# Optimization experiments

Hardware: AMD Instinct MI355X
Metric: run time of the kernel (lower is better)

Reference implementation:

```python
import jax, jax.numpy as jnp
import numpy as np

B, H, W = 8, 512, 512


def _focal_row_loss(logits, t):
    # logits: [B,2,H,W], t: [B,H,W] float. lossweight hardcoded to 1 as in source.
    logp = jax.nn.log_softmax(logits, axis=1)
    p = jnp.exp(logp)
    l = (-t * jnp.square(1.0 - p[:, 1]) * logp[:, 1]
         - (1.0 - t) * jnp.square(1.0 - p[:, 0]) * logp[:, 0])
    return l.reshape(l.shape[0], -1), p, logp


def _forward(inputs1, inputs2, inputs3, targets, forget_rate, kdweight):
    bsz = targets.shape[0]
    t = targets.astype(jnp.float32)
    loss_1, p1, lp1 = _focal_row_loss(inputs1, t)
    loss_2, p2, lp2 = _focal_row_loss(inputs2, t)
    loss_3, p3, lp3 = _focal_row_loss(inputs3, t)

    # symmetric per-pixel KL between the two class distributions (stable via log-softmax diff)
    kdl_12 = (p1[:, 0] * (lp1[:, 0] - lp2[:, 0]) + p1[:, 1] * (lp1[:, 1] - lp2[:, 1])).reshape(bsz, -1)
    kdl_21 = (p2[:, 0] * (lp2[:, 0] - lp1[:, 0]) + p2[:, 1] * (lp2[:, 1] - lp1[:, 1])).reshape(bsz, -1)

    loss = (1.0 - kdweight) * (loss_1 + loss_2 + loss_3) + kdweight * (kdl_12 + kdl_21)

    remember_rate = 1.0 - forget_rate
    num_remember = int(remember_rate * loss_1.shape[1])  # static: forget_rate is a Python float

    # on-device per-row top-(num_remember) smallest-loss pixels, then batched gather from loss_3
    ind_sorted = jnp.argsort(loss, axis=1)            # [B, N]
    ind_update = ind_sorted[:, :num_remember]          # [B, num_remember]
    loss_update = jnp.take_along_axis(loss_3, ind_update, axis=1)  # [B, num_remember]

    loss_out = jnp.mean(loss_update)  # reduction='mean'

    targets_s = t.reshape(bsz, -1)
    targets_sf = jnp.take_along_axis(targets_s, ind_update, axis=1)
    loss_s = targets_sf.sum() / t.sum()
    return loss_out, loss_s


def setup_inputs() -> dict:
    key = jax.random.key(0)
    k1, k2, k3, k4 = jax.random.split(key, 4)
    return {
        "inputs1": jax.random.normal(k1, (B, 2, H, W), dtype=jnp.float32),
        "inputs2": jax.random.normal(k2, (B, 2, H, W), dtype=jnp.float32),
        "inputs3": jax.random.normal(k3, (B, 2, H, W), dtype=jnp.float32),
        "targets": jax.random.randint(k4, (B, H, W), 0, 2, dtype=jnp.int32),
        "forget_rate": 0.2,
        "kdweight": 0.1,
    }


def reference(inputs1, inputs2, inputs3, targets, forget_rate, kdweight):
    return _forward(inputs1, inputs2, inputs3, targets, forget_rate, kdweight)
```

## Files before the change

kernel.cpp:

```cpp
#include <hip/hip_runtime.h>

#define NROWS  8
#define NPIX   262144
#define K1_BPR 256
#define KC_BPR 64
#define HB8    256
#define NSALT  16
#define SSTRIDE 257

__device__ __forceinline__ unsigned int fkey(float x){
  unsigned int u = __float_as_uint(x);
  return (u & 0x80000000u) ? ~u : (u | 0x80000000u);
}

__device__ __forceinline__ void softmax2(float a0, float a1,
    float& lp0, float& lp1, float& p0, float& p1){
  float d  = a1 - a0;
  float ad = -fabsf(d);
  float e  = __expf(ad);
  float s  = 1.0f + e;
  float ls = __logf(s);
  float rs = __builtin_amdgcn_rcpf(s);
  float lpM = -ls,  lpm = ad - ls;
  float pM  = rs,   pm  = e * rs;
  bool g = (d >= 0.0f);
  lp1 = g ? lpM : lpm;  lp0 = g ? lpm : lpM;
  p1  = g ? pM  : pm;   p0  = g ? pm  : pM;
}

__device__ __forceinline__ float focal2(float tt, float lp0, float lp1,
                                        float p0, float p1){
  float q1 = 1.0f - p1, q0 = 1.0f - p0;
  return -(tt * q1 * q1 * lp1) - ((1.0f - tt) * q0 * q0 * lp0);
}

__device__ __forceinline__ unsigned kTop(const float* frp){
  return (unsigned)((1.0 - (double)(*frp)) * (double)NPIX);
}

__device__ __forceinline__ uint2 selectBinV(unsigned v, unsigned kRem,
    unsigned* cum, unsigned* res){
  const int t = threadIdx.x;
  cum[t] = v;
  if (t == 0){ res[0] = 255u; res[1] = kRem; }
  __syncthreads();
  unsigned run = v;
  #pragma unroll
  for (int off = 1; off < 256; off <<= 1){
    unsigned add = (t >= off) ? cum[t - off] : 0u;
    __syncthreads();
    run += add;
    cum[t] = run;
    __syncthreads();
  }
  unsigned inc = cum[t], exc = inc - v;
  if (exc < kRem && inc >= kRem) { res[0] = (unsigned)t; res[1] = kRem - exc; }
  __syncthreads();
  uint2 r = make_uint2(res[0], res[1]);
  __syncthreads();
  return r;
}

__global__ __launch_bounds__(256) void k_compute(
    const float* __restrict__ in1, const float* __restrict__ in2,
    const float* __restrict__ in3, const int* __restrict__ tgt,
    const float* __restrict__ kdwp,
    unsigned int* __restrict__ packed, unsigned int* __restrict__ bhist16,
    unsigned int* __restrict__ gsub)
{
  __shared__ unsigned lh[NSALT * SSTRIDE];
  __shared__ unsigned lh2[HB8];
  const int t = threadIdx.x;
  for (int i = t; i < NSALT * SSTRIDE; i += 256) lh[i] = 0;

  const int blk   = blockIdx.x;
  const int row   = blk >> 8;
  const int chunk = (blk & (K1_BPR - 1)) * (NPIX / K1_BPR);
  const int base  = chunk + 4 * t;
  const float kdw = *kdwp;
  const float w1  = (float)(1.0 - (double)kdw);
  if (blk == 0){
    for (int i = t; i < 3 * NROWS * 16; i += 256) gsub[i] = 0u;
  }
  __syncthreads();

  const size_t ro2 = (size_t)row * 2 * NPIX;
  const size_t ro1 = (size_t)row * NPIX;

  float4 x10 = *(const float4*)(in1 + ro2 + base);
  float4 x11 = *(const float4*)(in1 + ro2 + NPIX + base);
  float4 x20 = *(const float4*)(in2 + ro2 + base);
  float4 x21 = *(const float4*)(in2 + ro2 + NPIX + base);
  float4 x30 = *(const float4*)(in3 + ro2 + base);
  float4 x31 = *(const float4*)(in3 + ro2 + NPIX + base);
  int4   tg  = *(const int4*)(tgt + ro1 + base);

  float a10[4] = {x10.x, x10.y, x10.z, x10.w};
  float a11[4] = {x11.x, x11.y, x11.z, x11.w};
  float a20[4] = {x20.x, x20.y, x20.z, x20.w};
  float a21[4] = {x21.x, x21.y, x21.z, x21.w};
  float a30[4] = {x30.x, x30.y, x30.z, x30.w};
  float a31[4] = {x31.x, x31.y, x31.z, x31.w};
  int   tgv[4] = {tg.x, tg.y, tg.z, tg.w};

  const int salt = (t & (NSALT - 1)) * SSTRIDE;
  unsigned pw[4];
  #pragma unroll
  for (int j = 0; j < 4; ++j){
    float tt = (float)tgv[j];
    float lp10, lp11, p10, p11; softmax2(a10[j], a11[j], lp10, lp11, p10, p11);
    float lp20, lp21, p20, p21; softmax2(a20[j], a21[j], lp20, lp21, p20, p21);
    float lp30, lp31, p30, p31; softmax2(a30[j], a31[j], lp30, lp31, p30, p31);
    float l1 = focal2(tt, lp10, lp11, p10, p11);
    float l2 = focal2(tt, lp20, lp21, p20, p21);
    float l3 = focal2(tt, lp30, lp31, p30, p31);
    float kdl12 = p10 * (lp10 - lp20) + p11 * (lp11 - lp21);
    float kdl21 = p20 * (lp20 - lp10) + p21 * (lp21 - lp11);
    float loss  = w1 * (l1 + l2 + l3) + kdw * (kdl12 + kdl21);
    unsigned k12 = fkey(loss) >> 20;
    unsigned lb = __float_as_uint(l3) + 0x1000u;
    pw[j] = (k12 << 20) | (((unsigned)tgv[j]) << 19) | ((lb >> 13) & 0x7FFFFu);
    atomicAdd(&lh[salt + (k12 >> 4)], 1u);
  }
  *(uint4*)(packed + ro1 + base) = make_uint4(pw[0], pw[1], pw[2], pw[3]);

  __syncthreads();
  unsigned v = 0;
  #pragma unroll
  for (int c = 0; c < NSALT; ++c) v += lh[c * SSTRIDE + t];
  lh2[t] = v;
  __syncthreads();
  if (t < HB8 / 2)
    bhist16[(size_t)blk * (HB8 / 2) + t] = lh2[2 * t] | (lh2[2 * t + 1] << 16);
}

__global__ __launch_bounds__(256) void k_collect(
    const unsigned int* __restrict__ packed,
    const unsigned int* __restrict__ bhist16,
    const float* __restrict__ frp,
    float* __restrict__ pB3, unsigned int* __restrict__ pBT,
    unsigned int* __restrict__ pAT,
    unsigned int* __restrict__ gsub, unsigned int* __restrict__ selKrem)
{
  __shared__ unsigned cum[256];
  __shared__ unsigned res[2];
  __shared__ unsigned lhw[4][HB8];
  __shared__ unsigned s_cnt[4][16];
  __shared__ float    s_l3[4][16];
  __shared__ unsigned s_tg[4][16];
  __shared__ float wf[4];
  __shared__ int   wi[8];
  const int t = threadIdx.x, lane = t & 63, wid = t >> 6;
  const int blk   = blockIdx.x;
  const int row   = blk >> 6;
  const int chunk = (blk & (KC_BPR - 1)) * (NPIX / KC_BPR);
  const size_t ro = (size_t)row * NPIX;
  if (t < 64){
    s_cnt[t >> 4][t & 15] = 0; s_l3[t >> 4][t & 15] = 0.0f;
    s_tg[t >> 4][t & 15] = 0;
  }

  const unsigned* bh = bhist16 + (size_t)row * K1_BPR * (HB8 / 2);
  unsigned s0a = 0, s1a = 0, s2a = 0, s3a = 0;
  #pragma unroll 8
  for (int i = 0; i < K1_BPR / 4; ++i){
    const unsigned* p = bh + (size_t)(wid + 4 * i) * (HB8 / 2) + 2 * lane;
    uint2 w2 = *(const uint2*)p;
    s0a += w2.x & 0xFFFFu; s1a += w2.x >> 16;
    s2a += w2.y & 0xFFFFu; s3a += w2.y >> 16;
  }
  *(uint4*)&lhw[wid][4 * lane] = make_uint4(s0a, s1a, s2a, s3a);
  __syncthreads();
  unsigned v = lhw[0][t] + lhw[1][t] + lhw[2][t] + lhw[3][t];

  uint2 s0 = selectBinV(v, kTop(frp), cum, res);
  const unsigned T8 = s0.x;
  if (t == 0) selKrem[row] = s0.y;

  float b3 = 0.0f; int bt = 0, at = 0;
  #pragma unroll
  for (int it = 0; it < 4; ++it){
    int base = chunk + it * 1024 + 4 * t;
    uint4 w = *(const uint4*)(packed + ro + base);
    unsigned a[4] = {w.x, w.y, w.z, w.w};
    #pragma unroll
    for (int j = 0; j < 4; ++j){
      unsigned k8 = a[j] >> 24;
      float l3 = __uint_as_float((a[j] & 0x7FFFFu) << 13);
      int   tv = (int)((a[j] >> 19) & 1u);
      at += tv;
      if (k8 < T8){ b3 += l3; bt += tv; }
      else if (k8 == T8){
        unsigned sub = (a[j] >> 20) & 15u;
        atomicAdd(&s_cnt[wid][sub], 1u);
        atomicAdd(&s_l3[wid][sub], l3);
        if (tv) atomicAdd(&s_tg[wid][sub], 1u);
      }
    }
  }
  #pragma unroll
  for (int o = 32; o; o >>= 1){
    b3 += __shfl_down(b3, o); bt += __shfl_down(bt, o); at += __shfl_down(at, o);
  }
  if (lane == 0){ wf[wid] = b3; wi[wid] = bt; wi[4 + wid] = at; }
  __syncthreads();
  if (t < 16){
    unsigned c = s_cnt[0][t] + s_cnt[1][t] + s_cnt[2][t] + s_cnt[3][t];
    float    l = s_l3[0][t] + s_l3[1][t] + s_l3[2][t] + s_l3[3][t];
    unsigned g = s_tg[0][t] + s_tg[1][t] + s_tg[2][t] + s_tg[3][t];
    if (c) atomicAdd(&gsub[row * 16 + t], c);
    if (l != 0.0f) atomicAdd((float*)&gsub[128 + row * 16 + t], l);
    if (g) atomicAdd(&gsub[256 + row * 16 + t], g);
  }
  if (t == 0){
    pB3[blk] = wf[0] + wf[1] + wf[2] + wf[3];
    pBT[blk] = (unsigned)(wi[0] + wi[1] + wi[2] + wi[3]);
    pAT[blk] = (unsigned)(wi[4] + wi[5] + wi[6] + wi[7]);
  }
}

__global__ __launch_bounds__(256) void k_final(
    const unsigned int* __restrict__ selKrem, const float* __restrict__ frp,
    const unsigned int* __restrict__ gsub,
    const float* __restrict__ pB3, const unsigned int* __restrict__ pBT,
    const unsigned int* __restrict__ pAT, float* __restrict__ out)
{
  __shared__ unsigned sh_sub[3 * NROWS * 16];
  __shared__ double dd[12];
  const int t = threadIdx.x, lane = t & 63, wid = t >> 6;
  const unsigned k0 = kTop(frp);
  for (int i = t; i < 3 * NROWS * 16; i += 256) sh_sub[i] = gsub[i];
  __syncthreads();

  double tie3 = 0.0, tieT = 0.0;
  if (t < NROWS){
    const int r = t;
    const unsigned kRem = selKrem[r];
    unsigned cum2 = 0;
    for (int s2 = 0; s2 < 16; ++s2){
      unsigned c = sh_sub[r * 16 + s2];
      if (c){
        unsigned take = 0;
        if (kRem > cum2){
          unsigned avail = kRem - cum2;
          take = (avail < c) ? avail : c;
        }
        if (take){
          double fr = (double)take / (double)c;
          tie3 += fr * (double)__uint_as_float(sh_sub[128 + r * 16 + s2]);
          tieT += fr * (double)sh_sub[256 + r * 16 + s2];
        }
        cum2 += c;
      }
    }
  }

  double S3 = tie3, ST = tieT, TT = 0.0;
  for (int i = t; i < NROWS * KC_BPR; i += 256){
    S3 += (double)pB3[i]; ST += (double)pBT[i]; TT += (double)pAT[i];
  }
  #pragma unroll
  for (int o = 32; o; o >>= 1){
    S3 += __shfl_down(S3, o); ST += __shfl_down(ST, o); TT += __shfl_down(TT, o);
  }
  if (lane == 0){ dd[wid] = S3; dd[4 + wid] = ST; dd[8 + wid] = TT; }
  __syncthreads();
  if (t == 0){
    double s0 = dd[0] + dd[1] + dd[2] + dd[3];
    double s1 = dd[4] + dd[5] + dd[6] + dd[7];
    double st = dd[8] + dd[9] + dd[10] + dd[11];
    out[0] = (float)(s0 / ((double)NROWS * (double)k0));
    out[1] = (float)(s1 / st);
  }
}

extern "C" void kernel_launch(void* const* d_in, const int* in_sizes, int n_in,
                              void* d_out, int out_size, void* d_ws, size_t ws_size,
                              hipStream_t stream)
{
  const float* in1  = (const float*)d_in[0];
  const float* in2  = (const float*)d_in[1];
  const float* in3  = (const float*)d_in[2];
  const int*   tgt  = (const int*)d_in[3];
  const float* frp  = (const float*)d_in[4];
  const float* kdwp = (const float*)d_in[5];
  float* out = (float*)d_out;
  char*  ws  = (char*)d_ws;

  const size_t off_packed = 0;
  const size_t off_bh16   = (size_t)NROWS * NPIX * 4;
  const size_t off_gsub   = off_bh16 + (size_t)NROWS * K1_BPR * (HB8/2) * 4;
  const size_t off_selKr  = off_gsub + 3 * NROWS * 16 * 4;
  const size_t off_pB3    = (off_selKr + NROWS * 4 + 255) & ~(size_t)255;
  const size_t off_pBT    = off_pB3 + (size_t)NROWS * KC_BPR * 4;
  const size_t off_pAT    = off_pBT + (size_t)NROWS * KC_BPR * 4;

  unsigned int* packed = (unsigned int*)(ws + off_packed);
  unsigned int* bh16   = (unsigned int*)(ws + off_bh16);
  unsigned int* gsub   = (unsigned int*)(ws + off_gsub);
  unsigned int* selKr  = (unsigned int*)(ws + off_selKr);
  float*        pB3    = (float*)(ws + off_pB3);
  unsigned int* pBT    = (unsigned int*)(ws + off_pBT);
  unsigned int* pAT    = (unsigned int*)(ws + off_pAT);

  k_compute<<<NROWS * K1_BPR, 256, 0, stream>>>(in1, in2, in3, tgt, kdwp,
                                                packed, bh16, gsub);
  k_collect<<<NROWS * KC_BPR, 256, 0, stream>>>(packed, bh16, frp,
                                                pB3, pBT, pAT, gsub, selKr);
  k_final<<<1, 256, 0, stream>>>(selKr, frp, gsub, pB3, pBT, pAT, out);
}
```

Before: 34.25 us.

## Use wave-shuffle prefix scan and per-thread LDS bins instead of shared atomics

The block-wide Hillis-Steele scan over 256 bins, which needed many __syncthreads, is replaced by a wavefront shuffle scan plus a small cross-wave prefix. Threshold-bin sub-histogram accumulation now writes per-thread private LDS slots instead of contended shared atomics, with count and target packed into one word, followed by a two-level tree reduction. This removes barriers and atomic contention in k_collect, at the cost of 32 KB of extra LDS, which could reduce occupancy, and extra reduction passes. The 16-bit packing limits the per-block count to under 65536.

```diff
diff --git a/kernel.cpp b/kernel.cpp
--- a/kernel.cpp
+++ b/kernel.cpp
@@ -36,29 +36,6 @@
 
 __device__ __forceinline__ unsigned kTop(const float* frp){
   return (unsigned)((1.0 - (double)(*frp)) * (double)NPIX);
-}
-
-__device__ __forceinline__ uint2 selectBinV(unsigned v, unsigned kRem,
-    unsigned* cum, unsigned* res){
-  const int t = threadIdx.x;
-  cum[t] = v;
-  if (t == 0){ res[0] = 255u; res[1] = kRem; }
-  __syncthreads();
-  unsigned run = v;
-  #pragma unroll
-  for (int off = 1; off < 256; off <<= 1){
-    unsigned add = (t >= off) ? cum[t - off] : 0u;
-    __syncthreads();
-    run += add;
-    cum[t] = run;
-    __syncthreads();
-  }
-  unsigned inc = cum[t], exc = inc - v;
-  if (exc < kRem && inc >= kRem) { res[0] = (unsigned)t; res[1] = kRem - exc; }
-  __syncthreads();
-  uint2 r = make_uint2(res[0], res[1]);
-  __syncthreads();
-  return r;
 }
 
 __global__ __launch_bounds__(256) void k_compute(
@@ -142,12 +119,11 @@
     unsigned int* __restrict__ pAT,
     unsigned int* __restrict__ gsub, unsigned int* __restrict__ selKrem)
 {
-  __shared__ unsigned cum[256];
+  __shared__ unsigned lhw[4][HB8];
+  __shared__ unsigned ct[16 * 256];
+  __shared__ float    sl[16 * 256];
+  __shared__ unsigned wsum[4];
   __shared__ unsigned res[2];
-  __shared__ unsigned lhw[4][HB8];
-  __shared__ unsigned s_cnt[4][16];
-  __shared__ float    s_l3[4][16];
-  __shared__ unsigned s_tg[4][16];
   __shared__ float wf[4];
   __shared__ int   wi[8];
   const int t = threadIdx.x, lane = t & 63, wid = t >> 6;
@@ -155,10 +131,9 @@
   const int row   = blk >> 6;
   const int chunk = (blk & (KC_BPR - 1)) * (NPIX / KC_BPR);
   const size_t ro = (size_t)row * NPIX;
-  if (t < 64){
-    s_cnt[t >> 4][t & 15] = 0; s_l3[t >> 4][t & 15] = 0.0f;
-    s_tg[t >> 4][t & 15] = 0;
-  }
+
+  #pragma unroll
+  for (int i = 0; i < 16; ++i){ ct[i * 256 + t] = 0u; sl[i * 256 + t] = 0.0f; }
 
   const unsigned* bh = bhist16 + (size_t)row * K1_BPR * (HB8 / 2);
   unsigned s0a = 0, s1a = 0, s2a = 0, s3a = 0;
@@ -170,12 +145,26 @@
     s2a += w2.y & 0xFFFFu; s3a += w2.y >> 16;
   }
   *(uint4*)&lhw[wid][4 * lane] = make_uint4(s0a, s1a, s2a, s3a);
+  const unsigned k0 = kTop(frp);
+  if (t == 0){ res[0] = 255u; res[1] = k0; }
   __syncthreads();
   unsigned v = lhw[0][t] + lhw[1][t] + lhw[2][t] + lhw[3][t];
 
-  uint2 s0 = selectBinV(v, kTop(frp), cum, res);
-  const unsigned T8 = s0.x;
-  if (t == 0) selKrem[row] = s0.y;
+  unsigned run = v;
+  #pragma unroll
+  for (int o = 1; o < 64; o <<= 1){
+    unsigned n = __shfl_up(run, o);
+    if (lane >= o) run += n;
+  }
+  if (lane == 63) wsum[wid] = run;
+  __syncthreads();
+  unsigned pre = 0;
+  for (int w = 0; w < 4; ++w) if (w < wid) pre += wsum[w];
+  unsigned inc = run + pre, exc = inc - v;
+  if (exc < k0 && inc >= k0){ res[0] = (unsigned)t; res[1] = k0 - exc; }
+  __syncthreads();
+  const unsigned T8 = res[0];
+  if (t == 0) selKrem[row] = res[1];
 
   float b3 = 0.0f; int bt = 0, at = 0;
   #pragma unroll
@@ -187,14 +176,13 @@
     for (int j = 0; j < 4; ++j){
       unsigned k8 = a[j] >> 24;
       float l3 = __uint_as_float((a[j] & 0x7FFFFu) << 13);
-      int   tv = (int)((a[j] >> 19) & 1u);
-      at += tv;
-      if (k8 < T8){ b3 += l3; bt += tv; }
+      unsigned tv = (a[j] >> 19) & 1u;
+      at += (int)tv;
+      if (k8 < T8){ b3 += l3; bt += (int)tv; }
       else if (k8 == T8){
-        unsigned sub = (a[j] >> 20) & 15u;
-        atomicAdd(&s_cnt[wid][sub], 1u);
-        atomicAdd(&s_l3[wid][sub], l3);
-        if (tv) atomicAdd(&s_tg[wid][sub], 1u);
+        int idx = (int)((a[j] >> 20) & 15u) * 256 + t;
+        ct[idx] += 1u | (tv << 16);
+        sl[idx] += l3;
       }
     }
   }
@@ -204,13 +192,30 @@
   }
   if (lane == 0){ wf[wid] = b3; wi[wid] = bt; wi[4 + wid] = at; }
   __syncthreads();
+
+  {
+    int s = t >> 4, c0 = (t & 15) * 16;
+    unsigned pc = 0; float pl = 0.0f;
+    #pragma unroll
+    for (int i = 0; i < 16; ++i){
+      pc += ct[s * 256 + c0 + i];
+      pl += sl[s * 256 + c0 + i];
+    }
+    lhw[0][t] = pc;
+    ((float*)lhw[1])[t] = pl;
+  }
+  __syncthreads();
   if (t < 16){
-    unsigned c = s_cnt[0][t] + s_cnt[1][t] + s_cnt[2][t] + s_cnt[3][t];
-    float    l = s_l3[0][t] + s_l3[1][t] + s_l3[2][t] + s_l3[3][t];
-    unsigned g = s_tg[0][t] + s_tg[1][t] + s_tg[2][t] + s_tg[3][t];
-    if (c) atomicAdd(&gsub[row * 16 + t], c);
-    if (l != 0.0f) atomicAdd((float*)&gsub[128 + row * 16 + t], l);
-    if (g) atomicAdd(&gsub[256 + row * 16 + t], g);
+    unsigned cc = 0; float ll = 0.0f;
+    #pragma unroll
+    for (int i = 0; i < 16; ++i){
+      cc += lhw[0][t * 16 + i];
+      ll += ((float*)lhw[1])[t * 16 + i];
+    }
+    unsigned cnt = cc & 0xFFFFu, tgc = cc >> 16;
+    if (cnt) atomicAdd(&gsub[row * 16 + t], cnt);
+    if (ll != 0.0f) atomicAdd((float*)&gsub[128 + row * 16 + t], ll);
+    if (tgc) atomicAdd(&gsub[256 + row * 16 + t], tgc);
   }
   if (t == 0){
     pB3[blk] = wf[0] + wf[1] + wf[2] + wf[3];
```

Measured after the change: 32.54 us (median of 2 runs). -5.0%, faster.
